# Optimization experiments

Measured on AMD Instinct MI355X. Metric: run time of the kernel, lower is better.

The kernel has to match this reference:

```python
import jax, jax.numpy as jnp
import numpy as np

B, L = 64, 512          # graphs, nodes per graph
N = B * L               # total nodes
INPUT_DIM, D, H, LAYERS, OUT = 128, 128, 8, 6, 10
DH = D // H
FF = 4 * D
E = 4 * N
SCALE = 0.02


def setup_inputs() -> dict:
    key = jax.random.key(0)
    ks = jax.random.split(key, 12)
    p = {}
    p['x'] = jax.random.normal(ks[0], (N, INPUT_DIM), jnp.float32)
    p['edge_index'] = jax.random.randint(ks[1], (2, E), 0, N, dtype=jnp.int64)
    p['batch'] = jnp.repeat(jnp.arange(B, dtype=jnp.int32), L)  # sorted graph ids
    p['max_nodes'] = L
    p['Wp'] = jax.random.normal(ks[2], (INPUT_DIM, D), jnp.float32) * SCALE
    p['bp'] = jnp.zeros((D,), jnp.float32)
    p['qkv_w'] = jax.random.normal(ks[3], (LAYERS, 3 * D, D), jnp.float32) * SCALE
    p['qkv_b'] = jnp.zeros((LAYERS, 3 * D), jnp.float32)
    p['out_w'] = jax.random.normal(ks[4], (LAYERS, D, D), jnp.float32) * SCALE
    p['out_b'] = jnp.zeros((LAYERS, D), jnp.float32)
    p['ln1_g'] = jnp.ones((LAYERS, D), jnp.float32)
    p['ln1_b'] = jnp.zeros((LAYERS, D), jnp.float32)
    p['ffn_w1'] = jax.random.normal(ks[5], (LAYERS, D, FF), jnp.float32) * SCALE
    p['ffn_b1'] = jnp.zeros((LAYERS, FF), jnp.float32)
    p['ffn_w2'] = jax.random.normal(ks[6], (LAYERS, FF, D), jnp.float32) * SCALE
    p['ffn_b2'] = jnp.zeros((LAYERS, D), jnp.float32)
    p['ln2_g'] = jnp.ones((LAYERS, D), jnp.float32)
    p['ln2_b'] = jnp.zeros((LAYERS, D), jnp.float32)
    p['cls_w1'] = jax.random.normal(ks[7], (D, D // 2), jnp.float32) * SCALE
    p['cls_b1'] = jnp.zeros((D // 2,), jnp.float32)
    p['cls_w2'] = jax.random.normal(ks[8], (D // 2, OUT), jnp.float32) * SCALE
    p['cls_b2'] = jnp.zeros((OUT,), jnp.float32)
    return p


def _ln(x, g, b, eps=1e-5):
    m = x.mean(-1, keepdims=True)
    v = ((x - m) ** 2).mean(-1, keepdims=True)
    return (x - m) * jax.lax.rsqrt(v + eps) * g + b


def _forward(x, batch, max_nodes, Wp, bp, qkv_w, qkv_b, out_w, out_b,
             ln1_g, ln1_b, ffn_w1, ffn_b1, ffn_w2, ffn_b2, ln2_g, ln2_b,
             cls_w1, cls_b1, cls_w2, cls_b2):
    n = x.shape[0]
    # --- vectorized ragged-to-dense (replaces the per-graph python loop) ---
    ones = jnp.ones((n,), jnp.int32)
    counts = jax.ops.segment_sum(ones, batch, num_segments=B)          # [B]
    starts = jnp.concatenate([jnp.zeros((1,), jnp.int32), jnp.cumsum(counts)[:-1]])
    pos = jnp.arange(n, dtype=jnp.int32) - starts[batch]               # slot within graph
    h0 = x @ Wp + bp                                                   # [N, D]
    h = jnp.zeros((B, max_nodes, D), h0.dtype).at[batch, pos].set(h0)  # [B, L, D]
    mask = jnp.zeros((B, max_nodes), bool).at[batch, pos].set(True)    # [B, L]
    # additive key-padding bias (src_key_padding_mask=~mask)
    bias = jnp.where(mask, 0.0, -1e9)[:, None, None, :]                # [B,1,1,L]
    inv_sqrt = 1.0 / np.sqrt(DH)
    for i in range(LAYERS):
        # --- post-norm MHA block ---
        qkv = jnp.einsum('bld,ed->ble', h, qkv_w[i]) + qkv_b[i]        # [B,L,3D]
        q, k, v = jnp.split(qkv, 3, axis=-1)
        q = q.reshape(B, max_nodes, H, DH).transpose(0, 2, 1, 3)       # [B,H,L,dh]
        k = k.reshape(B, max_nodes, H, DH).transpose(0, 2, 1, 3)
        v = v.reshape(B, max_nodes, H, DH).transpose(0, 2, 1, 3)
        scores = jnp.einsum('bhqd,bhkd->bhqk', q, k) * inv_sqrt + bias
        attn = jax.nn.softmax(scores, axis=-1)
        o = jnp.einsum('bhqk,bhkd->bhqd', attn, v)                     # [B,H,L,dh]
        o = o.transpose(0, 2, 1, 3).reshape(B, max_nodes, D)
        o = jnp.einsum('bld,ed->ble', o, out_w[i]) + out_b[i]
        h = _ln(h + o, ln1_g[i], ln1_b[i])
        # --- FFN block ---
        ff = jax.nn.relu(h @ ffn_w1[i] + ffn_b1[i]) @ ffn_w2[i] + ffn_b2[i]
        h = _ln(h + ff, ln2_g[i], ln2_b[i])
    # --- masked mean pooling per graph ---
    denom = jnp.maximum(counts.astype(h.dtype), 1.0)[:, None]          # [B,1]
    pooled = (h * mask[..., None].astype(h.dtype)).sum(axis=1) / denom # [B,D]
    # --- classifier head ---
    hid = jax.nn.relu(pooled @ cls_w1 + cls_b1)
    return hid @ cls_w2 + cls_b2                                       # [B,OUT]


def reference(x, edge_index, batch, max_nodes, Wp, bp, qkv_w, qkv_b, out_w, out_b,
              ln1_g, ln1_b, ffn_w1, ffn_b1, ffn_w2, ffn_b2, ln2_g, ln2_b,
              cls_w1, cls_b1, cls_w2, cls_b2):
    # edge_index is accepted (as in the torch module) but never used.
    return _forward(x, batch, max_nodes, Wp, bp, qkv_w, qkv_b, out_w, out_b,
                    ln1_g, ln1_b, ffn_w1, ffn_b1, ffn_w2, ffn_b2, ln2_g, ln2_b,
                    cls_w1, cls_b1, cls_w2, cls_b2)
```

## Files before the change

### kernel.cpp

```cpp
#include <hip/hip_runtime.h>
#include <hip/hip_bf16.h>


#define NROWS (64 * 512)
#define NLAYER 6

typedef __bf16 bf16x8 __attribute__((ext_vector_type(8)));
typedef float  f32x4  __attribute__((ext_vector_type(4)));
typedef float  f32x16 __attribute__((ext_vector_type(16)));

#define QSCALE 0.36067376022224085f

#if defined(__has_builtin)
#  if __has_builtin(__builtin_amdgcn_exp2f)
#    define FAST_EXP2(x) __builtin_amdgcn_exp2f(x)
#  endif
#endif
#ifndef FAST_EXP2
#  define FAST_EXP2(x) __expf((x) * 0.6931471805599453f)
#endif

__device__ __forceinline__ __hip_bfloat16 f2bf(float x) { return __float2bfloat16(x); }

__device__ __forceinline__ __hip_bfloat16 bf_rta(float a) {
  union { float f; unsigned u; } c{a};
  return __builtin_bit_cast(__hip_bfloat16, (unsigned short)((c.u + 0x8000u) >> 16));
}
__device__ __forceinline__ unsigned pk_rta(float a, float b) {
  union { float f; unsigned u; } ca{a}, cb{b};
  return ((ca.u + 0x8000u) >> 16) | ((cb.u + 0x8000u) & 0xFFFF0000u);
}
__device__ __forceinline__ float bf_hi(unsigned u) {
  return __builtin_bit_cast(float, u & 0xFFFF0000u);
}
__device__ __forceinline__ float bf_lo(unsigned u) {
  return __builtin_bit_cast(float, u << 16);
}

#define PN_X   (NROWS * 128)
#define PN_WP  (128 * 128)
#define PN_QW  (6 * 384 * 128)
#define PN_QB  (6 * 384)
#define PN_OW  (6 * 128 * 128)
#define PN_W1  (6 * 128 * 512)
#define PN_W2  (6 * 512 * 128)
#define PB1 PN_X
#define PB2 (PB1 + PN_WP)
#define PB3 (PB2 + PN_QW)
#define PB4 (PB3 + PN_QB)
#define PB5 (PB4 + PN_OW)
#define PB6 (PB5 + PN_W1)
#define PB7 (PB6 + PN_W2)

__global__ __launch_bounds__(256) void prep_kernel(
    const float* __restrict__ x, __hip_bfloat16* __restrict__ xb,
    const float* __restrict__ Wp, __hip_bfloat16* __restrict__ wp_t,
    const float* __restrict__ qkv_w, __hip_bfloat16* __restrict__ qkvw,
    const float* __restrict__ qkv_b, float* __restrict__ qb_s,
    const float* __restrict__ out_w, __hip_bfloat16* __restrict__ outw,
    const float* __restrict__ ffn_w1, __hip_bfloat16* __restrict__ w1t,
    const float* __restrict__ ffn_w2, __hip_bfloat16* __restrict__ w2t)
{
  const int idx = blockIdx.x * 256 + threadIdx.x;
  if (idx < PB1) {
    xb[idx] = f2bf(x[idx]);
  } else if (idx < PB2) {
    const int i = idx - PB1;
    const int c = i >> 7, r = i & 127;
    wp_t[i] = f2bf(Wp[r * 128 + c]);
  } else if (idx < PB3) {
    const int i = idx - PB2;
    const int row = (i >> 7) % 384;
    qkvw[i] = f2bf(qkv_w[i] * ((row < 128) ? QSCALE : 1.f));
  } else if (idx < PB4) {
    const int i = idx - PB3;
    qb_s[i] = qkv_b[i] * (((i % 384) < 128) ? QSCALE : 1.f);
  } else if (idx < PB5) {
    const int i = idx - PB4;
    outw[i] = f2bf(out_w[i]);
  } else if (idx < PB6) {
    const int i = idx - PB5;
    const int l = i >> 16, j = i & 65535;
    const int c = j >> 7, r = j & 127;
    w1t[i] = f2bf(ffn_w1[l * 65536 + r * 512 + c]);
  } else if (idx < PB7) {
    const int i = idx - PB6;
    const int l = i >> 16, j = i & 65535;
    const int c = j >> 9, r = j & 511;
    w2t[i] = f2bf(ffn_w2[l * 65536 + r * 128 + c]);
  }
}

__global__ __launch_bounds__(256) void gemm_fk(
    const __hip_bfloat16* __restrict__ A, const __hip_bfloat16* __restrict__ B,
    const float* __restrict__ bias, __hip_bfloat16* __restrict__ outb,
    __hip_bfloat16* __restrict__ hb,
    const float* __restrict__ lng, const float* __restrict__ lnb,
    int M, int K, int flags)
{
  __shared__ __align__(16) __hip_bfloat16 As[64 * 136];
  __shared__ __align__(16) __hip_bfloat16 Bs[128 * 136];

  const int tid = threadIdx.x;
  const int m0 = blockIdx.x << 6;
  const int wave = tid >> 6;
  const int lane = tid & 63;
  const int quad = lane >> 4;
  const int l15 = lane & 15;
  const int wrow = wave * 16;

  f32x4 acc[8];
#pragma unroll
  for (int ni = 0; ni < 8; ++ni) acc[ni] = (f32x4){0.f, 0.f, 0.f, 0.f};

  for (int kc = 0; kc < K; kc += 128) {
#pragma unroll
    for (int p = 0; p < 4; ++p) {
      const int e = tid + (p << 8);
      const int row = e >> 4;
      const int c = e & 15;
      *(uint4*)&As[row * 136 + c * 8] =
          *(const uint4*)(A + (size_t)(m0 + row) * K + kc + c * 8);
    }
#pragma unroll
    for (int p = 0; p < 8; ++p) {
      const int e = tid + (p << 8);
      const int row = e >> 4;
      const int c = e & 15;
      *(uint4*)&Bs[row * 136 + c * 8] =
          *(const uint4*)(B + (size_t)row * K + kc + c * 8);
    }
    __syncthreads();

#pragma unroll
    for (int ks = 0; ks < 4; ++ks) {
      const bf16x8 af = *(const bf16x8*)&As[(wrow + l15) * 136 + ks * 32 + quad * 8];
#pragma unroll
      for (int ni = 0; ni < 8; ++ni) {
        const bf16x8 bfr =
            *(const bf16x8*)&Bs[(ni * 16 + l15) * 136 + ks * 32 + quad * 8];
        acc[ni] = __builtin_amdgcn_mfma_f32_16x16x32_bf16(af, bfr, acc[ni], 0, 0, 0);
      }
    }
    if (kc + 128 < K) __syncthreads();
  }

  if (flags & 2) {
#pragma unroll
    for (int r = 0; r < 4; ++r) {
      const size_t row = (size_t)(m0 + wrow + quad * 4 + r);
      float s = 0.f, sq = 0.f;
#pragma unroll
      for (int ni = 0; ni < 8; ++ni) {
        const int cl = ni * 16 + l15;
        const float v = acc[ni][r] + bias[cl] +
                        __bfloat162float(hb[row * 128 + cl]);
        acc[ni][r] = v;
        s += v;
        sq += v * v;
      }
#pragma unroll
      for (int off = 1; off <= 8; off <<= 1) {
        s += __shfl_xor(s, off, 64);
        sq += __shfl_xor(sq, off, 64);
      }
      const float mean = s * (1.f / 128.f);
      const float var = sq * (1.f / 128.f) - mean * mean;
      const float rs = rsqrtf(var + 1e-5f);
#pragma unroll
      for (int ni = 0; ni < 8; ++ni) {
        const int cl = ni * 16 + l15;
        const float o = (acc[ni][r] - mean) * rs * lng[cl] + lnb[cl];
        hb[row * 128 + cl] = bf_rta(o);
      }
    }
  } else {
#pragma unroll
    for (int ni = 0; ni < 8; ++ni) {
      const int cl = ni * 16 + l15;
      const float bv = bias[cl];
#pragma unroll
      for (int r = 0; r < 4; ++r) {
        float v = acc[ni][r] + bv;
        if (flags & 1) v = fmaxf(v, 0.f);
        outb[(size_t)(m0 + wrow + quad * 4 + r) * 128 + cl] = bf_rta(v);
      }
    }
  }
}

__global__ __launch_bounds__(256) void oproj_ffn(
    const __hip_bfloat16* __restrict__ ab,
    __hip_bfloat16* __restrict__ hb,
    const __hip_bfloat16* __restrict__ ow,
    const float* __restrict__ ob,
    const float* __restrict__ ln1g, const float* __restrict__ ln1b,
    const __hip_bfloat16* __restrict__ w1,
    const __hip_bfloat16* __restrict__ w2,
    const float* __restrict__ fb1, const float* __restrict__ fb2,
    const float* __restrict__ ln2g, const float* __restrict__ ln2b)
{
  __shared__ __align__(16) __hip_bfloat16 AF[64 * 136];
  __shared__ __align__(16) __hip_bfloat16 Bs[128 * 136];

  const int tid = threadIdx.x;
  const int m0 = blockIdx.x << 6;
  const int wave = tid >> 6;
  const int lane = tid & 63;
  const int quad = lane >> 4;
  const int l15 = lane & 15;
  const int wrow = wave * 16;
  const int node = m0 + wrow + l15;
  const int ch0 = quad * 4;

  uint2 hres[8];
#pragma unroll
  for (int ni = 0; ni < 8; ++ni)
    hres[ni] = *(const uint2*)(hb + (size_t)node * 128 + ni * 16 + ch0);

#pragma unroll
  for (int p = 0; p < 4; ++p) {
    const int e = tid + (p << 8);
    const int row = e >> 4, c = e & 15;
    *(uint4*)&AF[row * 136 + c * 8] =
        *(const uint4*)(ab + (size_t)(m0 + row) * 128 + c * 8);
  }
#pragma unroll
  for (int p = 0; p < 8; ++p) {
    const int e = tid + (p << 8);
    const int row = e >> 4, c = e & 15;
    *(uint4*)&Bs[row * 136 + c * 8] =
        *(const uint4*)(ow + (size_t)row * 128 + c * 8);
  }
  __syncthreads();

  bf16x8 af[4];
#pragma unroll
  for (int ks = 0; ks < 4; ++ks)
    af[ks] = *(const bf16x8*)&AF[(wrow + l15) * 136 + ks * 32 + quad * 8];

  f32x4 acc[8];
#pragma unroll
  for (int ni = 0; ni < 8; ++ni) acc[ni] = (f32x4){0.f, 0.f, 0.f, 0.f};
#pragma unroll
  for (int ks = 0; ks < 4; ++ks)
#pragma unroll
    for (int ni = 0; ni < 8; ++ni) {
      const bf16x8 bfr =
          *(const bf16x8*)&Bs[(ni * 16 + l15) * 136 + ks * 32 + quad * 8];
      acc[ni] = __builtin_amdgcn_mfma_f32_16x16x32_bf16(bfr, af[ks], acc[ni], 0, 0, 0);
    }

  {
    float s = 0.f, sq = 0.f;
#pragma unroll
    for (int ni = 0; ni < 8; ++ni) {
      const f32x4 obv = *(const f32x4*)(ob + ni * 16 + ch0);
#pragma unroll
      for (int r = 0; r < 4; ++r) {
        const unsigned hu = (r & 2) ? hres[ni].y : hres[ni].x;
        const float hv = (r & 1) ? bf_hi(hu) : bf_lo(hu);
        const float v = acc[ni][r] + obv[r] + hv;
        acc[ni][r] = v;
        s += v;
        sq += v * v;
      }
    }
    s += __shfl_xor(s, 16, 64);  sq += __shfl_xor(sq, 16, 64);
    s += __shfl_xor(s, 32, 64);  sq += __shfl_xor(sq, 32, 64);
    const float mean = s * (1.f / 128.f);
    const float rs = rsqrtf(sq * (1.f / 128.f) - mean * mean + 1e-5f);
#pragma unroll
    for (int ni = 0; ni < 8; ++ni) {
      const f32x4 gv = *(const f32x4*)(ln1g + ni * 16 + ch0);
      const f32x4 bv = *(const f32x4*)(ln1b + ni * 16 + ch0);
      const float o0 = (acc[ni][0] - mean) * rs * gv[0] + bv[0];
      const float o1 = (acc[ni][1] - mean) * rs * gv[1] + bv[1];
      const float o2 = (acc[ni][2] - mean) * rs * gv[2] + bv[2];
      const float o3 = (acc[ni][3] - mean) * rs * gv[3] + bv[3];
      const uint2 pk = make_uint2(pk_rta(o0, o1), pk_rta(o2, o3));
      hres[ni] = pk;
      *(uint2*)&AF[(wrow + l15) * 136 + ni * 16 + ch0] = pk;
    }
  }

  __syncthreads();
#pragma unroll
  for (int p = 0; p < 8; ++p) {
    const int e = tid + (p << 8);
    const int row = e >> 4, cc = e & 15;
    *(uint4*)&Bs[row * 136 + cc * 8] =
        *(const uint4*)(w1 + (size_t)row * 128 + cc * 8);
  }
  bf16x8 hf[4];
#pragma unroll
  for (int ks = 0; ks < 4; ++ks)
    hf[ks] = *(const bf16x8*)&AF[(wrow + l15) * 136 + ks * 32 + quad * 8];
  __syncthreads();

  f32x4 facc[8];
#pragma unroll
  for (int ni = 0; ni < 8; ++ni) facc[ni] = (f32x4){0.f, 0.f, 0.f, 0.f};

  for (int c = 0; c < 4; ++c) {
    if (c > 0) {
      __syncthreads();
#pragma unroll
      for (int p = 0; p < 8; ++p) {
        const int e = tid + (p << 8);
        const int row = e >> 4, cc = e & 15;
        *(uint4*)&Bs[row * 136 + cc * 8] =
            *(const uint4*)(w1 + (size_t)(c * 128 + row) * 128 + cc * 8);
      }
      __syncthreads();
    }

    f32x4 fc[8];
#pragma unroll
    for (int ni = 0; ni < 8; ++ni) fc[ni] = (f32x4){0.f, 0.f, 0.f, 0.f};
#pragma unroll
    for (int ks = 0; ks < 4; ++ks)
#pragma unroll
      for (int ni = 0; ni < 8; ++ni) {
        const bf16x8 wf =
            *(const bf16x8*)&Bs[(ni * 16 + l15) * 136 + ks * 32 + quad * 8];
        fc[ni] = __builtin_amdgcn_mfma_f32_16x16x32_bf16(wf, hf[ks], fc[ni], 0, 0, 0);
      }
#pragma unroll
    for (int ni = 0; ni < 8; ++ni) {
      const f32x4 bv = *(const f32x4*)(fb1 + c * 128 + ni * 16 + ch0);
      const float v0 = fmaxf(fc[ni][0] + bv[0], 0.f);
      const float v1 = fmaxf(fc[ni][1] + bv[1], 0.f);
      const float v2 = fmaxf(fc[ni][2] + bv[2], 0.f);
      const float v3 = fmaxf(fc[ni][3] + bv[3], 0.f);
      *(uint2*)&AF[(wrow + l15) * 136 + ni * 16 + ch0] =
          make_uint2(pk_rta(v0, v1), pk_rta(v2, v3));
    }
    __syncthreads();

#pragma unroll
    for (int p = 0; p < 8; ++p) {
      const int e = tid + (p << 8);
      const int row = e >> 4, cc = e & 15;
      *(uint4*)&Bs[row * 136 + cc * 8] =
          *(const uint4*)(w2 + (size_t)row * 512 + c * 128 + cc * 8);
    }
    __syncthreads();

#pragma unroll
    for (int ks2 = 0; ks2 < 4; ++ks2) {
      const bf16x8 ff =
          *(const bf16x8*)&AF[(wrow + l15) * 136 + ks2 * 32 + quad * 8];
#pragma unroll
      for (int ni = 0; ni < 8; ++ni) {
        const bf16x8 wf =
            *(const bf16x8*)&Bs[(ni * 16 + l15) * 136 + ks2 * 32 + quad * 8];
        facc[ni] = __builtin_amdgcn_mfma_f32_16x16x32_bf16(wf, ff, facc[ni], 0, 0, 0);
      }
    }
  }

  {
    float s = 0.f, sq = 0.f;
#pragma unroll
    for (int ni = 0; ni < 8; ++ni) {
      const f32x4 b2v = *(const f32x4*)(fb2 + ni * 16 + ch0);
#pragma unroll
      for (int r = 0; r < 4; ++r) {
        const unsigned hu = (r & 2) ? hres[ni].y : hres[ni].x;
        const float hv = (r & 1) ? bf_hi(hu) : bf_lo(hu);
        const float v = facc[ni][r] + b2v[r] + hv;
        facc[ni][r] = v;
        s += v;
        sq += v * v;
      }
    }
    s += __shfl_xor(s, 16, 64);  sq += __shfl_xor(sq, 16, 64);
    s += __shfl_xor(s, 32, 64);  sq += __shfl_xor(sq, 32, 64);
    const float mean = s * (1.f / 128.f);
    const float rs = rsqrtf(sq * (1.f / 128.f) - mean * mean + 1e-5f);
#pragma unroll
    for (int ni = 0; ni < 8; ++ni) {
      const f32x4 gv = *(const f32x4*)(ln2g + ni * 16 + ch0);
      const f32x4 bv = *(const f32x4*)(ln2b + ni * 16 + ch0);
      const float o0 = (facc[ni][0] - mean) * rs * gv[0] + bv[0];
      const float o1 = (facc[ni][1] - mean) * rs * gv[1] + bv[1];
      const float o2 = (facc[ni][2] - mean) * rs * gv[2] + bv[2];
      const float o3 = (facc[ni][3] - mean) * rs * gv[3] + bv[3];
      *(uint2*)(hb + (size_t)node * 128 + ni * 16 + ch0) =
          make_uint2(pk_rta(o0, o1), pk_rta(o2, o3));
    }
  }
}

__global__ __launch_bounds__(512) void attn_kernel(
    const __hip_bfloat16* __restrict__ hbf,
    const __hip_bfloat16* __restrict__ qkvw_l,
    const float* __restrict__ qb_l,
    __hip_bfloat16* __restrict__ o)
{
  __shared__ __align__(16) __hip_bfloat16 Ks[512 * 16];
  __shared__ __align__(16) __hip_bfloat16 Vt[16 * 520];
  __shared__ __align__(16) __hip_bfloat16 PQ[8][2048];

  const int tid = threadIdx.x;
  const int b = blockIdx.x & 63;
  const int hh = blockIdx.x >> 6;
  const __hip_bfloat16* hrow = hbf + (size_t)b * 512 * 128;

  const int wave = tid >> 6;
  const int lane = tid & 63;
  const int l31 = lane & 31;
  const int l5 = lane >> 5;
  const int l15 = lane & 15;
  const int quad = lane >> 4;
  const int q0 = wave * 64;

  {
    f32x4 qacc[4], kacc[4], vacc[4];
#pragma unroll
    for (int mt = 0; mt < 4; ++mt) {
      qacc[mt] = (f32x4){0.f, 0.f, 0.f, 0.f};
      kacc[mt] = (f32x4){0.f, 0.f, 0.f, 0.f};
      vacc[mt] = (f32x4){0.f, 0.f, 0.f, 0.f};
    }
#pragma unroll
    for (int ks = 0; ks < 4; ++ks) {
      const int kc = ks * 32 + quad * 8;
      const bf16x8 wq = *(const bf16x8*)(qkvw_l + (size_t)(hh * 16 + l15) * 128 + kc);
      const bf16x8 wk = *(const bf16x8*)(qkvw_l + (size_t)(128 + hh * 16 + l15) * 128 + kc);
      const bf16x8 wv = *(const bf16x8*)(qkvw_l + (size_t)(256 + hh * 16 + l15) * 128 + kc);
#pragma unroll
      for (int mt = 0; mt < 4; ++mt) {
        const bf16x8 hf =
            *(const bf16x8*)(hrow + (size_t)(q0 + mt * 16 + l15) * 128 + kc);
        qacc[mt] = __builtin_amdgcn_mfma_f32_16x16x32_bf16(wq, hf, qacc[mt], 0, 0, 0);
        kacc[mt] = __builtin_amdgcn_mfma_f32_16x16x32_bf16(wk, hf, kacc[mt], 0, 0, 0);
        vacc[mt] = __builtin_amdgcn_mfma_f32_16x16x32_bf16(hf, wv, vacc[mt], 0, 0, 0);
      }
    }
    const f32x4 qbv = *(const f32x4*)(qb_l + hh * 16 + quad * 4);
    const f32x4 kbv = *(const f32x4*)(qb_l + 128 + hh * 16 + quad * 4);
    const float vbs = qb_l[256 + hh * 16 + l15];
#pragma unroll
    for (int mt = 0; mt < 4; ++mt) {
      {
        const int qrow = mt * 16 + l15;
        const int qg = (quad >> 1) ^ ((qrow >> 1) & 3);
        *(uint2*)&PQ[wave][qrow * 32 + qg * 8 + (quad & 1) * 4] =
            make_uint2(pk_rta(qacc[mt][0] + qbv[0], qacc[mt][1] + qbv[1]),
                       pk_rta(qacc[mt][2] + qbv[2], qacc[mt][3] + qbv[3]));
      }
      {
        const int krow = q0 + mt * 16 + l15;
        const int ke = (krow * 16 + quad * 4) ^ ((l15 & 7) << 3);
        *(uint2*)&Ks[ke] =
            make_uint2(pk_rta(kacc[mt][0] + kbv[0], kacc[mt][1] + kbv[1]),
                       pk_rta(kacc[mt][2] + kbv[2], kacc[mt][3] + kbv[3]));
      }
      *(uint2*)&Vt[l15 * 520 + q0 + mt * 16 + quad * 4] =
          make_uint2(pk_rta(vacc[mt][0] + vbs, vacc[mt][1] + vbs),
                     pk_rta(vacc[mt][2] + vbs, vacc[mt][3] + vbs));
    }
  }

  bf16x8 qf[2];
#pragma unroll
  for (int s = 0; s < 2; ++s)
    qf[s] = *(const bf16x8*)
        &PQ[wave][(s * 32 + l31) * 32 + (l5 ^ ((l31 >> 1) & 3)) * 8];
  __syncthreads();

  __hip_bfloat16* Pw = &PQ[wave][0];
  const f32x16 z16 = {};
  f32x4 oacc[2][2];
#pragma unroll
  for (int s = 0; s < 2; ++s) { oacc[s][0] = (f32x4){0.f,0.f,0.f,0.f};
                                oacc[s][1] = (f32x4){0.f,0.f,0.f,0.f}; }
  float lacc[2] = {0.f, 0.f};

  const int psw = (l31 >> 1) & 3;
  const int prs = (l15 >> 1) & 3;

  const int kbase = (l31 * 16 + l5 * 8) ^ ((l31 & 7) << 3);

  bf16x8 kf = *(const bf16x8*)&Ks[kbase];
  f32x16 st0 = __builtin_amdgcn_mfma_f32_32x32x16_bf16(kf, qf[0], z16, 0, 0, 0);

  for (int kt = 0; kt < 16; ++kt) {
    const bf16x8 vf = *(const bf16x8*)&Vt[l15 * 520 + kt * 32 + quad * 8];

    {
      float pr[16];
#pragma unroll
      for (int r = 0; r < 16; ++r) pr[r] = FAST_EXP2(st0[r]);
      const float a0 = (pr[0] + pr[1]) + (pr[2] + pr[3]);
      const float a1 = (pr[4] + pr[5]) + (pr[6] + pr[7]);
      const float a2 = (pr[8] + pr[9]) + (pr[10] + pr[11]);
      const float a3 = (pr[12] + pr[13]) + (pr[14] + pr[15]);
      lacc[0] += (a0 + a1) + (a2 + a3);
#pragma unroll
      for (int g = 0; g < 4; ++g) {
        *(uint2*)&Pw[l31 * 32 + ((g ^ psw)) * 8 + l5 * 4] =
            make_uint2(pk_rta(pr[g * 4 + 0], pr[g * 4 + 1]),
                       pk_rta(pr[g * 4 + 2], pr[g * 4 + 3]));
      }
    }
    f32x16 st1 = __builtin_amdgcn_mfma_f32_32x32x16_bf16(kf, qf[1], z16, 0, 0, 0);
#pragma unroll
    for (int g = 0; g < 2; ++g) {
      const bf16x8 pf =
          *(const bf16x8*)&Pw[(g * 16 + l15) * 32 + ((quad ^ prs)) * 8];
      oacc[0][g] = __builtin_amdgcn_mfma_f32_16x16x32_bf16(vf, pf, oacc[0][g], 0, 0, 0);
    }

    {
      float pr[16];
#pragma unroll
      for (int r = 0; r < 16; ++r) pr[r] = FAST_EXP2(st1[r]);
      const float a0 = (pr[0] + pr[1]) + (pr[2] + pr[3]);
      const float a1 = (pr[4] + pr[5]) + (pr[6] + pr[7]);
      const float a2 = (pr[8] + pr[9]) + (pr[10] + pr[11]);
      const float a3 = (pr[12] + pr[13]) + (pr[14] + pr[15]);
      lacc[1] += (a0 + a1) + (a2 + a3);
#pragma unroll
      for (int g = 0; g < 4; ++g) {
        *(uint2*)&Pw[l31 * 32 + ((g ^ psw)) * 8 + l5 * 4] =
            make_uint2(pk_rta(pr[g * 4 + 0], pr[g * 4 + 1]),
                       pk_rta(pr[g * 4 + 2], pr[g * 4 + 3]));
      }
    }
    if (kt < 15) {
      kf = *(const bf16x8*)&Ks[(kt + 1) * 512 + kbase];
      st0 = __builtin_amdgcn_mfma_f32_32x32x16_bf16(kf, qf[0], z16, 0, 0, 0);
    }
#pragma unroll
    for (int g = 0; g < 2; ++g) {
      const bf16x8 pf =
          *(const bf16x8*)&Pw[(g * 16 + l15) * 32 + ((quad ^ prs)) * 8];
      oacc[1][g] = __builtin_amdgcn_mfma_f32_16x16x32_bf16(vf, pf, oacc[1][g], 0, 0, 0);
    }
  }

#pragma unroll
  for (int s = 0; s < 2; ++s) {
    const float lv = lacc[s] + __shfl_xor(lacc[s], 32, 64);
#pragma unroll
    for (int g = 0; g < 2; ++g) {
      const float lq = __shfl(lv, g * 16 + l15, 64);
      const float inv = 1.f / lq;
      const int qrow = q0 + s * 32 + g * 16 + l15;
      *(uint2*)(o + ((size_t)b * 512 + qrow) * 128 + hh * 16 + quad * 4) =
          make_uint2(pk_rta(oacc[s][g][0] * inv, oacc[s][g][1] * inv),
                     pk_rta(oacc[s][g][2] * inv, oacc[s][g][3] * inv));
    }
  }
}

__global__ __launch_bounds__(256) void head_kernel(
    const __hip_bfloat16* __restrict__ h,
    const float* __restrict__ w1, const float* __restrict__ b1,
    const float* __restrict__ w2, const float* __restrict__ b2,
    float* __restrict__ out)
{
  __shared__ float part[2][128];
  __shared__ float pooled[128];
  __shared__ float hid[64];

  const int b = blockIdx.x;
  const int tid = threadIdx.x;
  const int d = tid & 127;
  const int half = tid >> 7;

  const __hip_bfloat16* hp = h + ((size_t)b * 512 + (size_t)half * 256) * 128;
  float s = 0.f;
  for (int r = 0; r < 256; ++r) s += __bfloat162float(hp[(size_t)r * 128 + d]);
  part[half][d] = s;
  __syncthreads();

  if (tid < 128) pooled[tid] = (part[0][tid] + part[1][tid]) * (1.f / 512.f);
  __syncthreads();

  if (tid < 64) {
    float a = b1[tid];
    for (int dd = 0; dd < 128; ++dd) a = fmaf(pooled[dd], w1[dd * 64 + tid], a);
    hid[tid] = fmaxf(a, 0.f);
  }
  __syncthreads();

  if (tid < 10) {
    float a = b2[tid];
    for (int j = 0; j < 64; ++j) a = fmaf(hid[j], w2[j * 10 + tid], a);
    out[b * 10 + tid] = a;
  }
}

extern "C" void kernel_launch(void* const* d_in, const int* in_sizes, int n_in,
                              void* d_out, int out_size, void* d_ws, size_t ws_size,
                              hipStream_t stream)
{
  (void)in_sizes; (void)n_in; (void)out_size; (void)ws_size;

  const float* x      = (const float*)d_in[0];
  const float* Wp     = (const float*)d_in[4];
  const float* bp     = (const float*)d_in[5];
  const float* qkv_w  = (const float*)d_in[6];
  const float* qkv_b  = (const float*)d_in[7];
  const float* out_w  = (const float*)d_in[8];
  const float* out_b  = (const float*)d_in[9];
  const float* ln1_g  = (const float*)d_in[10];
  const float* ln1_b  = (const float*)d_in[11];
  const float* ffn_w1 = (const float*)d_in[12];
  const float* ffn_b1 = (const float*)d_in[13];
  const float* ffn_w2 = (const float*)d_in[14];
  const float* ffn_b2 = (const float*)d_in[15];
  const float* ln2_g  = (const float*)d_in[16];
  const float* ln2_b  = (const float*)d_in[17];
  const float* cw1    = (const float*)d_in[18];
  const float* cb1    = (const float*)d_in[19];
  const float* cw2    = (const float*)d_in[20];
  const float* cb2    = (const float*)d_in[21];

  const int N = NROWS;

  __hip_bfloat16* hbf   = (__hip_bfloat16*)d_ws;
  __hip_bfloat16* xb    = hbf + (size_t)N * 128;
  __hip_bfloat16* attnb = xb + (size_t)N * 128;
  __hip_bfloat16* wp_t  = attnb + (size_t)N * 128;
  __hip_bfloat16* qkvw  = wp_t + 128 * 128;
  __hip_bfloat16* outw  = qkvw + 6 * 384 * 128;
  __hip_bfloat16* w1t   = outw + 6 * 128 * 128;
  __hip_bfloat16* w2t   = w1t + 6 * 512 * 128;
  float* qb_s = (float*)(w2t + 6 * 128 * 512);

  const dim3 blk(256);
  __hip_bfloat16* const nob = (__hip_bfloat16*)nullptr;
  const float* const nof = (const float*)nullptr;

  prep_kernel<<<dim3((PB7 + 255) / 256), blk, 0, stream>>>(
      x, xb, Wp, wp_t, qkv_w, qkvw, qkv_b, qb_s, out_w, outw,
      ffn_w1, w1t, ffn_w2, w2t);

  gemm_fk<<<dim3(N / 64), blk, 0, stream>>>(
      xb, wp_t, bp, hbf, nob, nof, nof, N, 128, 0);

  for (int i = 0; i < NLAYER; ++i) {
    attn_kernel<<<dim3(64 * 8), dim3(512), 0, stream>>>(
        hbf, qkvw + (size_t)i * 384 * 128, qb_s + (size_t)i * 384, attnb);

    oproj_ffn<<<dim3(N / 64), blk, 0, stream>>>(
        attnb, hbf,
        outw + (size_t)i * 128 * 128, out_b + (size_t)i * 128,
        ln1_g + (size_t)i * 128, ln1_b + (size_t)i * 128,
        w1t + (size_t)i * 512 * 128, w2t + (size_t)i * 128 * 512,
        ffn_b1 + (size_t)i * 512, ffn_b2 + (size_t)i * 128,
        ln2_g + (size_t)i * 128, ln2_b + (size_t)i * 128);
  }

  head_kernel<<<dim3(64), blk, 0, stream>>>(hbf, cw1, cb1, cw2, cb2, (float*)d_out);
}
```

Before: 489.5 us.

## Keep softmax probabilities in registers via permlane32 swap instead of LDS round-trip

The P·V step in attention now feeds the 32x32x16 MFMA directly from registers. Lanes exchange packed bf16 probability values with v_permlane32_swap, which replaces the old path of writing P to shared memory and reading it back for 16x16x32 MFMAs. V is loaded in a new fragment layout. Because half the output columns are duplicated and predicated off, the epilogue now writes scalar bf16 values with per-row shuffles. This trades LDS traffic and latency for wasted MFMA work, since only 16 of the 32 columns are useful, and a less coalesced output store.

```diff
diff --git a/kernel.cpp b/kernel.cpp
--- a/kernel.cpp
+++ b/kernel.cpp
@@ -35,6 +35,14 @@
 }
 __device__ __forceinline__ float bf_lo(unsigned u) {
   return __builtin_bit_cast(float, u << 16);
+}
+__device__ __forceinline__ void plswap(unsigned &a, unsigned &b) {
+  asm volatile("v_permlane32_swap_b32 %0, %1" : "+v"(a), "+v"(b));
+}
+__device__ __forceinline__ bf16x8 mk_bf8(unsigned u0, unsigned u1,
+                                         unsigned u2, unsigned u3) {
+  uint4 t; t.x = u0; t.y = u1; t.z = u2; t.w = u3;
+  return __builtin_bit_cast(bf16x8, t);
 }
 
 #define PN_X   (NROWS * 128)
@@ -471,25 +479,23 @@
         &PQ[wave][(s * 32 + l31) * 32 + (l5 ^ ((l31 >> 1) & 3)) * 8];
   __syncthreads();
 
-  __hip_bfloat16* Pw = &PQ[wave][0];
   const f32x16 z16 = {};
-  f32x4 oacc[2][2];
-#pragma unroll
-  for (int s = 0; s < 2; ++s) { oacc[s][0] = (f32x4){0.f,0.f,0.f,0.f};
-                                oacc[s][1] = (f32x4){0.f,0.f,0.f,0.f}; }
+  f32x16 oacc[2];
+  oacc[0] = z16;
+  oacc[1] = z16;
   float lacc[2] = {0.f, 0.f};
 
-  const int psw = (l31 >> 1) & 3;
-  const int prs = (l15 >> 1) & 3;
-
   const int kbase = (l31 * 16 + l5 * 8) ^ ((l31 & 7) << 3);
+  const int vrow = (l31 & 15) * 520;
 
   bf16x8 kf = *(const bf16x8*)&Ks[kbase];
   f32x16 st0 = __builtin_amdgcn_mfma_f32_32x32x16_bf16(kf, qf[0], z16, 0, 0, 0);
 
   for (int kt = 0; kt < 16; ++kt) {
-    const bf16x8 vf = *(const bf16x8*)&Vt[l15 * 520 + kt * 32 + quad * 8];
-
+    const bf16x8 vb1 = *(const bf16x8*)&Vt[vrow + kt * 32 + l5 * 8];
+    const bf16x8 vb2 = *(const bf16x8*)&Vt[vrow + kt * 32 + 16 + l5 * 8];
+
+    bf16x8 f1a, f2a;
     {
       float pr[16];
 #pragma unroll
@@ -499,21 +505,20 @@
       const float a2 = (pr[8] + pr[9]) + (pr[10] + pr[11]);
       const float a3 = (pr[12] + pr[13]) + (pr[14] + pr[15]);
       lacc[0] += (a0 + a1) + (a2 + a3);
-#pragma unroll
-      for (int g = 0; g < 4; ++g) {
-        *(uint2*)&Pw[l31 * 32 + ((g ^ psw)) * 8 + l5 * 4] =
-            make_uint2(pk_rta(pr[g * 4 + 0], pr[g * 4 + 1]),
-                       pk_rta(pr[g * 4 + 2], pr[g * 4 + 3]));
-      }
+      unsigned c0 = pk_rta(pr[0], pr[1]),  c1 = pk_rta(pr[2], pr[3]);
+      unsigned c2 = pk_rta(pr[4], pr[5]),  c3 = pk_rta(pr[6], pr[7]);
+      unsigned c4 = pk_rta(pr[8], pr[9]),  c5 = pk_rta(pr[10], pr[11]);
+      unsigned c6 = pk_rta(pr[12], pr[13]), c7 = pk_rta(pr[14], pr[15]);
+      plswap(c0, c2); plswap(c1, c3);
+      plswap(c4, c6); plswap(c5, c7);
+      f1a = mk_bf8(c0, c1, c2, c3);
+      f2a = mk_bf8(c4, c5, c6, c7);
     }
     f32x16 st1 = __builtin_amdgcn_mfma_f32_32x32x16_bf16(kf, qf[1], z16, 0, 0, 0);
-#pragma unroll
-    for (int g = 0; g < 2; ++g) {
-      const bf16x8 pf =
-          *(const bf16x8*)&Pw[(g * 16 + l15) * 32 + ((quad ^ prs)) * 8];
-      oacc[0][g] = __builtin_amdgcn_mfma_f32_16x16x32_bf16(vf, pf, oacc[0][g], 0, 0, 0);
-    }
-
+    oacc[0] = __builtin_amdgcn_mfma_f32_32x32x16_bf16(f1a, vb1, oacc[0], 0, 0, 0);
+    oacc[0] = __builtin_amdgcn_mfma_f32_32x32x16_bf16(f2a, vb2, oacc[0], 0, 0, 0);
+
+    bf16x8 f1b, f2b;
     {
       float pr[16];
 #pragma unroll
@@ -523,36 +528,35 @@
       const float a2 = (pr[8] + pr[9]) + (pr[10] + pr[11]);
       const float a3 = (pr[12] + pr[13]) + (pr[14] + pr[15]);
       lacc[1] += (a0 + a1) + (a2 + a3);
-#pragma unroll
-      for (int g = 0; g < 4; ++g) {
-        *(uint2*)&Pw[l31 * 32 + ((g ^ psw)) * 8 + l5 * 4] =
-            make_uint2(pk_rta(pr[g * 4 + 0], pr[g * 4 + 1]),
-                       pk_rta(pr[g * 4 + 2], pr[g * 4 + 3]));
-      }
+      unsigned c0 = pk_rta(pr[0], pr[1]),  c1 = pk_rta(pr[2], pr[3]);
+      unsigned c2 = pk_rta(pr[4], pr[5]),  c3 = pk_rta(pr[6], pr[7]);
+      unsigned c4 = pk_rta(pr[8], pr[9]),  c5 = pk_rta(pr[10], pr[11]);
+      unsigned c6 = pk_rta(pr[12], pr[13]), c7 = pk_rta(pr[14], pr[15]);
+      plswap(c0, c2); plswap(c1, c3);
+      plswap(c4, c6); plswap(c5, c7);
+      f1b = mk_bf8(c0, c1, c2, c3);
+      f2b = mk_bf8(c4, c5, c6, c7);
     }
     if (kt < 15) {
       kf = *(const bf16x8*)&Ks[(kt + 1) * 512 + kbase];
       st0 = __builtin_amdgcn_mfma_f32_32x32x16_bf16(kf, qf[0], z16, 0, 0, 0);
     }
-#pragma unroll
-    for (int g = 0; g < 2; ++g) {
-      const bf16x8 pf =
-          *(const bf16x8*)&Pw[(g * 16 + l15) * 32 + ((quad ^ prs)) * 8];
-      oacc[1][g] = __builtin_amdgcn_mfma_f32_16x16x32_bf16(vf, pf, oacc[1][g], 0, 0, 0);
-    }
+    oacc[1] = __builtin_amdgcn_mfma_f32_32x32x16_bf16(f1b, vb1, oacc[1], 0, 0, 0);
+    oacc[1] = __builtin_amdgcn_mfma_f32_32x32x16_bf16(f2b, vb2, oacc[1], 0, 0, 0);
   }
 
 #pragma unroll
   for (int s = 0; s < 2; ++s) {
     const float lv = lacc[s] + __shfl_xor(lacc[s], 32, 64);
-#pragma unroll
-    for (int g = 0; g < 2; ++g) {
-      const float lq = __shfl(lv, g * 16 + l15, 64);
-      const float inv = 1.f / lq;
-      const int qrow = q0 + s * 32 + g * 16 + l15;
-      *(uint2*)(o + ((size_t)b * 512 + qrow) * 128 + hh * 16 + quad * 4) =
-          make_uint2(pk_rta(oacc[s][g][0] * inv, oacc[s][g][1] * inv),
-                     pk_rta(oacc[s][g][2] * inv, oacc[s][g][3] * inv));
+    const float inv_own = 1.f / lv;
+#pragma unroll
+    for (int r = 0; r < 16; ++r) {
+      const int qrow = (r & 3) + 8 * (r >> 2) + 4 * l5;
+      const float linv = __shfl(inv_own, qrow, 64);
+      if (l31 < 16) {
+        o[((size_t)b * 512 + q0 + s * 32 + qrow) * 128 + hh * 16 + l31] =
+            bf_rta(oacc[s][r] * linv);
+      }
     }
   }
 }
```

Result: slower. 502.7 us (+2.7%).
